# Kernel tuning notes

Measured on AMD Instinct MI355X. Metric: run time of the kernel, lower is better.

Reference implementation:

```python
import jax, jax.numpy as jnp
import numpy as np

N = 100000   # nodes
E = 1600000  # edges (avg degree 16)
F_IN = 64
H = 64
C = 40       # classes


def setup_inputs() -> dict:
    key = jax.random.key(0)
    ks = jax.random.split(key, 12)

    def lin(k, out_d, in_d):
        kw, kb = jax.random.split(k)
        W = jax.random.normal(kw, (out_d, in_d), jnp.float32) / jnp.sqrt(jnp.float32(in_d))
        b = jnp.zeros((out_d,), jnp.float32)
        return W, b

    Wl1, b1 = lin(ks[2], H, F_IN)
    Wr1, _ = lin(ks[3], H, F_IN)
    Wl2, b2 = lin(ks[4], H, H)
    Wr2, _ = lin(ks[5], H, H)
    Wl3, b3 = lin(ks[6], C, H)
    Wr3, _ = lin(ks[7], C, H)

    return {
        "x": jax.random.normal(ks[0], (N, F_IN), jnp.float32),
        "edge_index": jax.random.randint(ks[1], (2, E), 0, N, jnp.int32),
        "Wl1": Wl1, "Wr1": Wr1, "b1": b1,
        "Wl2": Wl2, "Wr2": Wr2, "b2": b2,
        "Wl3": Wl3, "Wr3": Wr3, "b3": b3,
    }


def _sage_conv(x, src, dst, Wl, Wr, b, n_nodes):
    # PyG SAGEConv (aggr='mean'): out = lin_l(mean_{j in N(i)} x_j) + lin_r(x_i)
    msg = x[src]                                                   # [E, F] gather
    agg_sum = jax.ops.segment_sum(msg, dst, num_segments=n_nodes)  # [N, F]
    deg = jax.ops.segment_sum(jnp.ones((src.shape[0],), x.dtype), dst,
                              num_segments=n_nodes)                # [N]
    agg = agg_sum / jnp.maximum(deg, 1.0)[:, None]                 # mean aggregation
    return agg @ Wl.T + b + x @ Wr.T


def reference(x, edge_index, Wl1, Wr1, b1, Wl2, Wr2, b2, Wl3, Wr3, b3):
    src, dst = edge_index[0], edge_index[1]
    n = x.shape[0]
    # dropout is identity in eval mode (training=self.training)
    h = jax.nn.relu(_sage_conv(x, src, dst, Wl1, Wr1, b1, n))
    h = jax.nn.relu(_sage_conv(h, src, dst, Wl2, Wr2, b2, n))
    h = _sage_conv(h, src, dst, Wl3, Wr3, b3, n)
    return jax.nn.log_softmax(h, axis=1)
```

## Files before the change

kernel.cpp:

```cpp
#include <hip/hip_runtime.h>
#include <hip/hip_bf16.h>
#include <math.h>


#define BK_SHIFT 7
#define BK_NODES 128
#define NB_MAX   1024

typedef __attribute__((ext_vector_type(8))) short short8;
typedef __attribute__((ext_vector_type(4))) float f32x4;

__device__ inline float blo(unsigned v) { union { unsigned u; float f; } c; c.u = v << 16; return c.f; }
__device__ inline float bhi(unsigned v) { union { unsigned u; float f; } c; c.u = v & 0xFFFF0000u; return c.f; }
__device__ inline unsigned short f2bf(float f) {
    union { float f; unsigned u; } c; c.f = f;
    unsigned r = (c.u + 0x7FFFu + ((c.u >> 16) & 1u)) >> 16;
    return (unsigned short)r;
}

__global__ __launch_bounds__(256) void bcount_kernel(const int* __restrict__ dstA,
                                                     int* __restrict__ bcount, int E, int NB) {
    __shared__ int lc[NB_MAX];
    int t = threadIdx.x;
    for (int i = t; i < NB; i += 256) lc[i] = 0;
    __syncthreads();
    int step = gridDim.x * 256;
    for (int e = blockIdx.x * 256 + t; e < E; e += step)
        atomicAdd(&lc[dstA[e] >> BK_SHIFT], 1);
    __syncthreads();
    for (int i = t; i < NB; i += 256)
        if (lc[i]) atomicAdd(&bcount[i], lc[i]);
}

__global__ __launch_bounds__(1024) void bscan_kernel(const int* __restrict__ bcount,
                                                     int* __restrict__ bbase,
                                                     int* __restrict__ cursor, int NB, int E) {
    __shared__ int s[1024];
    int t = threadIdx.x;
    int v = (t < NB) ? bcount[t] : 0;
    s[t] = v;
    __syncthreads();
    for (int off = 1; off < 1024; off <<= 1) {
        int x = 0;
        if (t >= off) x = s[t - off];
        __syncthreads();
        s[t] += x;
        __syncthreads();
    }
    if (t < NB) {
        int ex = s[t] - v;
        bbase[t] = ex;
        cursor[t] = ex;
    }
    if (t == 0) bbase[NB] = E;
}

__global__ __launch_bounds__(256) void bin_kernel(const int* __restrict__ srcA,
                                                  const int* __restrict__ dstA,
                                                  int* __restrict__ cursor,
                                                  int* __restrict__ binned, int E, int NB) {
    __shared__ int lc[NB_MAX];
    __shared__ int lbase[NB_MAX];
    int t = threadIdx.x;
    int chunk = (E + gridDim.x - 1) / gridDim.x;
    int e0 = blockIdx.x * chunk;
    int e1 = min(E, e0 + chunk);
    for (int i = t; i < NB; i += 256) lc[i] = 0;
    __syncthreads();
    for (int e = e0 + t; e < e1; e += 256)
        atomicAdd(&lc[dstA[e] >> BK_SHIFT], 1);
    __syncthreads();
    for (int i = t; i < NB; i += 256) {
        int c = lc[i];
        lbase[i] = c ? atomicAdd(&cursor[i], c) : 0;
    }
    __syncthreads();
    for (int i = t; i < NB; i += 256) lc[i] = 0;
    __syncthreads();
    for (int e = e0 + t; e < e1; e += 256) {
        int d = dstA[e];
        int b = d >> BK_SHIFT;
        int r = atomicAdd(&lc[b], 1);
        binned[lbase[b] + r] = srcA[e] | ((d & (BK_NODES - 1)) << 24);
    }
}

__global__ __launch_bounds__(256) void bsort_kernel(const int* __restrict__ binned,
                                                    const int* __restrict__ bbase,
                                                    int* __restrict__ col,
                                                    int* __restrict__ row_start, int N) {
    __shared__ int cnt[BK_NODES];
    __shared__ int base[BK_NODES];
    __shared__ int s[BK_NODES];
    int b = blockIdx.x, t = threadIdx.x;
    int e0 = bbase[b], e1 = bbase[b + 1];
    if (t < BK_NODES) cnt[t] = 0;
    __syncthreads();
    for (int e = e0 + t; e < e1; e += 256)
        atomicAdd(&cnt[(unsigned)binned[e] >> 24], 1);
    __syncthreads();
    int v = (t < BK_NODES) ? cnt[t] : 0;
    if (t < BK_NODES) s[t] = v;
    __syncthreads();
    for (int off = 1; off < BK_NODES; off <<= 1) {
        int x = 0;
        if (t < BK_NODES && t >= off) x = s[t - off];
        __syncthreads();
        if (t < BK_NODES) s[t] += x;
        __syncthreads();
    }
    if (t < BK_NODES) {
        base[t] = e0 + s[t] - v;
        int node = b * BK_NODES + t;
        if (node < N) row_start[node] = base[t];
        cnt[t] = 0;
    }
    if (b == gridDim.x - 1 && t == 0) row_start[N] = e1;
    __syncthreads();
    for (int e = e0 + t; e < e1; e += 256) {
        unsigned p = (unsigned)binned[e];
        int dl = p >> 24;
        int pos = base[dl] + atomicAdd(&cnt[dl], 1);
        col[pos] = p & 0xFFFFFF;
    }
}

__global__ __launch_bounds__(256) void xconv_kernel(const float* __restrict__ x,
                                                    unsigned short* __restrict__ Xb, int n8) {
    int i = blockIdx.x * 256 + threadIdx.x;
    if (i >= n8) return;
    const float* p = x + (size_t)i * 8;
    float4 a = *(const float4*)p;
    float4 b = *(const float4*)(p + 4);
    uint4 o;
    o.x = f2bf(a.x) | ((unsigned)f2bf(a.y) << 16);
    o.y = f2bf(a.z) | ((unsigned)f2bf(a.w) << 16);
    o.z = f2bf(b.x) | ((unsigned)f2bf(b.y) << 16);
    o.w = f2bf(b.z) | ((unsigned)f2bf(b.w) << 16);
    *(uint4*)(Xb + (size_t)i * 8) = o;
}

__global__ __launch_bounds__(256) void wconv_kernel(const float* __restrict__ Wl1, const float* __restrict__ Wr1,
                                                    const float* __restrict__ Wl2, const float* __restrict__ Wr2,
                                                    const float* __restrict__ Wl3, const float* __restrict__ Wr3,
                                                    unsigned short* __restrict__ Wb1,
                                                    unsigned short* __restrict__ Wb2,
                                                    unsigned short* __restrict__ Wb3) {
    int i = blockIdx.x * 256 + threadIdx.x;
    if (i < 8192) {
        int c = i >> 7, k = i & 127;
        float v = (k < 64) ? Wl1[c * 64 + k] : Wr1[c * 64 + k - 64];
        Wb1[i] = f2bf(v);
    } else if (i < 16384) {
        int j = i - 8192;
        int c = j >> 7, k = j & 127;
        float v = (k < 64) ? Wl2[c * 64 + k] : Wr2[c * 64 + k - 64];
        Wb2[j] = f2bf(v);
    } else if (i < 22528) {
        int j = i - 16384;
        int c = j >> 6, k = j & 63;
        float v = 0.f;
        if (c < 40) v = Wl3[c * 64 + k];
        else if (c >= 48 && c < 88) v = Wr3[(c - 48) * 64 + k];
        Wb3[j] = f2bf(v);
    }
}

__global__ __launch_bounds__(256) void agg64_kernel(const unsigned short* __restrict__ X,
                                                    const int* __restrict__ rs,
                                                    const int* __restrict__ col,
                                                    unsigned short* __restrict__ OUT, int n) {
    int t = threadIdx.x;
    int node = blockIdx.x * 16 + (t >> 4);
    if (node >= n) return;
    int lane = t & 15;
    int s = rs[node], d = rs[node + 1] - s;
    const unsigned short* lp = X + lane * 4;
    float ax = 0.f, ay = 0.f, az = 0.f, aw = 0.f;
    int j = 0;
    for (; j + 3 < d; j += 4) {
        int c0 = col[s + j], c1 = col[s + j + 1];
        int c2 = col[s + j + 2], c3 = col[s + j + 3];
        uint2 q0 = *(const uint2*)(lp + (size_t)c0 * 64);
        uint2 q1 = *(const uint2*)(lp + (size_t)c1 * 64);
        uint2 q2 = *(const uint2*)(lp + (size_t)c2 * 64);
        uint2 q3 = *(const uint2*)(lp + (size_t)c3 * 64);
        ax += (blo(q0.x) + blo(q1.x)) + (blo(q2.x) + blo(q3.x));
        ay += (bhi(q0.x) + bhi(q1.x)) + (bhi(q2.x) + bhi(q3.x));
        az += (blo(q0.y) + blo(q1.y)) + (blo(q2.y) + blo(q3.y));
        aw += (bhi(q0.y) + bhi(q1.y)) + (bhi(q2.y) + bhi(q3.y));
    }
    for (; j < d; ++j) {
        int c0 = col[s + j];
        uint2 q0 = *(const uint2*)(lp + (size_t)c0 * 64);
        ax += blo(q0.x); ay += bhi(q0.x); az += blo(q0.y); aw += bhi(q0.y);
    }
    float w = 1.f / (float)(d > 0 ? d : 1);
    ax *= w; ay *= w; az *= w; aw *= w;
    uint2 o;
    o.x = f2bf(ax) | ((unsigned)f2bf(ay) << 16);
    o.y = f2bf(az) | ((unsigned)f2bf(aw) << 16);
    *(uint2*)(OUT + (size_t)node * 64 + lane * 4) = o;
}

__global__ __launch_bounds__(256) void linmfma12_kernel(const unsigned short* __restrict__ A,
                                                        const unsigned short* __restrict__ X,
                                                        const unsigned short* __restrict__ Wb,
                                                        const float* __restrict__ bias,
                                                        unsigned short* __restrict__ OUT,
                                                        int N) {
    __shared__ unsigned short Ys[64][136];
    __shared__ unsigned short Ws[64][136];
    int t = threadIdx.x;
    int rowbase = blockIdx.x * 64;
#pragma unroll
    for (int it = 0; it < 4; ++it) {
        int idx = it * 256 + t;
        int row = idx >> 4, c = idx & 15;
        int grow = rowbase + row;
        if (grow >= N) grow = N - 1;
        const unsigned short* src = (c < 8) ? (A + (size_t)grow * 64 + c * 8)
                                            : (X + (size_t)grow * 64 + (c - 8) * 8);
        *(short8*)&Ys[row][c * 8] = *(const short8*)src;
        *(short8*)&Ws[row][c * 8] = *(const short8*)(Wb + (size_t)row * 128 + c * 8);
    }
    __syncthreads();
    int l = t & 63, w = t >> 6;
    int lrow = l & 15, lk = l >> 4;
    f32x4 acc0 = {0.f, 0.f, 0.f, 0.f};
    f32x4 acc1 = acc0, acc2 = acc0, acc3 = acc0;
#pragma unroll
    for (int kk = 0; kk < 4; ++kk) {
        int ko = kk * 32 + lk * 8;
        short8 a  = *(const short8*)&Ys[16 * w + lrow][ko];
        short8 b0 = *(const short8*)&Ws[lrow][ko];
        short8 b1 = *(const short8*)&Ws[16 + lrow][ko];
        short8 b2 = *(const short8*)&Ws[32 + lrow][ko];
        short8 b3 = *(const short8*)&Ws[48 + lrow][ko];
        acc0 = __builtin_amdgcn_mfma_f32_16x16x32_bf16(a, b0, acc0, 0, 0, 0);
        acc1 = __builtin_amdgcn_mfma_f32_16x16x32_bf16(a, b1, acc1, 0, 0, 0);
        acc2 = __builtin_amdgcn_mfma_f32_16x16x32_bf16(a, b2, acc2, 0, 0, 0);
        acc3 = __builtin_amdgcn_mfma_f32_16x16x32_bf16(a, b3, acc3, 0, 0, 0);
    }
#define EPI12(nt, accv)                                                   \
    {                                                                     \
        int colc = 16 * (nt) + lrow;                                      \
        float bv = bias[colc];                                            \
        _Pragma("unroll") for (int i = 0; i < 4; ++i) {                   \
            int grow = rowbase + 16 * w + lk * 4 + i;                     \
            if (grow < N) {                                               \
                float v = fmaxf(accv[i] + bv, 0.f);                       \
                OUT[(size_t)grow * 64 + colc] = f2bf(v);                  \
            }                                                             \
        }                                                                 \
    }
    EPI12(0, acc0) EPI12(1, acc1) EPI12(2, acc2) EPI12(3, acc3)
#undef EPI12
}

__global__ __launch_bounds__(256) void linmfma3_kernel(const unsigned short* __restrict__ H,
                                                       const unsigned short* __restrict__ Wb3,
                                                       const float* __restrict__ b3,
                                                       unsigned short* __restrict__ Z,
                                                       float* __restrict__ R,
                                                       int N) {
    __shared__ unsigned short Ys[64][72];
    __shared__ unsigned short Ws[96][72];
    int t = threadIdx.x;
    int rowbase = blockIdx.x * 64;
#pragma unroll
    for (int it = 0; it < 2; ++it) {
        int idx = it * 256 + t;
        int row = idx >> 3, c = idx & 7;
        int grow = rowbase + row;
        if (grow >= N) grow = N - 1;
        *(short8*)&Ys[row][c * 8] = *(const short8*)(H + (size_t)grow * 64 + c * 8);
    }
#pragma unroll
    for (int it = 0; it < 3; ++it) {
        int idx = it * 256 + t;
        int row = idx >> 3, c = idx & 7;
        *(short8*)&Ws[row][c * 8] = *(const short8*)(Wb3 + (size_t)row * 64 + c * 8);
    }
    __syncthreads();
    int l = t & 63, w = t >> 6;
    int lrow = l & 15, lk = l >> 4;
    f32x4 acc0 = {0.f, 0.f, 0.f, 0.f};
    f32x4 acc1 = acc0, acc2 = acc0, acc3 = acc0, acc4 = acc0, acc5 = acc0;
#pragma unroll
    for (int kk = 0; kk < 2; ++kk) {
        int ko = kk * 32 + lk * 8;
        short8 a  = *(const short8*)&Ys[16 * w + lrow][ko];
        short8 b0 = *(const short8*)&Ws[lrow][ko];
        short8 b1 = *(const short8*)&Ws[16 + lrow][ko];
        short8 b2 = *(const short8*)&Ws[32 + lrow][ko];
        short8 b3f = *(const short8*)&Ws[48 + lrow][ko];
        short8 b4 = *(const short8*)&Ws[64 + lrow][ko];
        short8 b5 = *(const short8*)&Ws[80 + lrow][ko];
        acc0 = __builtin_amdgcn_mfma_f32_16x16x32_bf16(a, b0, acc0, 0, 0, 0);
        acc1 = __builtin_amdgcn_mfma_f32_16x16x32_bf16(a, b1, acc1, 0, 0, 0);
        acc2 = __builtin_amdgcn_mfma_f32_16x16x32_bf16(a, b2, acc2, 0, 0, 0);
        acc3 = __builtin_amdgcn_mfma_f32_16x16x32_bf16(a, b3f, acc3, 0, 0, 0);
        acc4 = __builtin_amdgcn_mfma_f32_16x16x32_bf16(a, b4, acc4, 0, 0, 0);
        acc5 = __builtin_amdgcn_mfma_f32_16x16x32_bf16(a, b5, acc5, 0, 0, 0);
    }
#define EPI3(nt, accv)                                                     \
    {                                                                      \
        int colc = 16 * (nt) + lrow;                                       \
        _Pragma("unroll") for (int i = 0; i < 4; ++i) {                    \
            int grow = rowbase + 16 * w + lk * 4 + i;                      \
            if (grow < N) {                                                \
                float v = accv[i];                                         \
                if (colc < 40) {                                           \
                    Z[(size_t)grow * 40 + colc] = f2bf(v);                 \
                } else if (colc >= 48 && colc < 88) {                      \
                    R[(size_t)grow * 40 + (colc - 48)] = v + b3[colc - 48];\
                }                                                          \
            }                                                              \
        }                                                                  \
    }
    EPI3(0, acc0) EPI3(1, acc1) EPI3(2, acc2) EPI3(3, acc3) EPI3(4, acc4) EPI3(5, acc5)
#undef EPI3
}

__global__ __launch_bounds__(256) void agg40lsm_kernel(const unsigned short* __restrict__ Z,
                                                       const int* __restrict__ rs,
                                                       const int* __restrict__ col,
                                                       float* __restrict__ out, int n) {
    int t = threadIdx.x;
    int node = blockIdx.x * 16 + (t >> 4);
    if (node >= n) return;
    int lane = t & 15;
    bool act = lane < 10;
    int s = rs[node], d = rs[node + 1] - s;
    const unsigned short* lp = Z + lane * 4;
    float ax = 0.f, ay = 0.f, az = 0.f, aw = 0.f;
    int j = 0;
    for (; j + 3 < d; j += 4) {
        int c0 = col[s + j], c1 = col[s + j + 1];
        int c2 = col[s + j + 2], c3 = col[s + j + 3];
        if (act) {
            uint2 q0 = *(const uint2*)(lp + (size_t)c0 * 40);
            uint2 q1 = *(const uint2*)(lp + (size_t)c1 * 40);
            uint2 q2 = *(const uint2*)(lp + (size_t)c2 * 40);
            uint2 q3 = *(const uint2*)(lp + (size_t)c3 * 40);
            ax += (blo(q0.x) + blo(q1.x)) + (blo(q2.x) + blo(q3.x));
            ay += (bhi(q0.x) + bhi(q1.x)) + (bhi(q2.x) + bhi(q3.x));
            az += (blo(q0.y) + blo(q1.y)) + (blo(q2.y) + blo(q3.y));
            aw += (bhi(q0.y) + bhi(q1.y)) + (bhi(q2.y) + bhi(q3.y));
        }
    }
    for (; j < d; ++j) {
        int c0 = col[s + j];
        if (act) {
            uint2 q0 = *(const uint2*)(lp + (size_t)c0 * 40);
            ax += blo(q0.x); ay += bhi(q0.x); az += blo(q0.y); aw += bhi(q0.y);
        }
    }
    float w = 1.f / (float)(d > 0 ? d : 1);
    if (act) {
        float4 rv = *(const float4*)(out + (size_t)node * 40 + lane * 4);
        ax = ax * w + rv.x; ay = ay * w + rv.y;
        az = az * w + rv.z; aw = aw * w + rv.w;
    }
    float mx = act ? fmaxf(fmaxf(ax, ay), fmaxf(az, aw)) : -3.4e38f;
#pragma unroll
    for (int off = 1; off < 16; off <<= 1) mx = fmaxf(mx, __shfl_xor(mx, off, 16));
    float ssum = act ? (expf(ax - mx) + expf(ay - mx) + expf(az - mx) + expf(aw - mx)) : 0.f;
#pragma unroll
    for (int off = 1; off < 16; off <<= 1) ssum += __shfl_xor(ssum, off, 16);
    float lg = mx + logf(ssum);
    if (act) {
        float4 o;
        o.x = ax - lg; o.y = ay - lg; o.z = az - lg; o.w = aw - lg;
        *(float4*)(out + (size_t)node * 40 + lane * 4) = o;
    }
}

extern "C" void kernel_launch(void* const* d_in, const int* in_sizes, int n_in,
                              void* d_out, int out_size, void* d_ws, size_t ws_size,
                              hipStream_t stream) {
    const float* x   = (const float*)d_in[0];
    const int*   ei  = (const int*)d_in[1];
    const float* Wl1 = (const float*)d_in[2];
    const float* Wr1 = (const float*)d_in[3];
    const float* b1  = (const float*)d_in[4];
    const float* Wl2 = (const float*)d_in[5];
    const float* Wr2 = (const float*)d_in[6];
    const float* b2  = (const float*)d_in[7];
    const float* Wl3 = (const float*)d_in[8];
    const float* Wr3 = (const float*)d_in[9];
    const float* b3  = (const float*)d_in[10];
    float* out = (float*)d_out;

    const int N = in_sizes[0] / 64;
    const int E = in_sizes[1] / 2;
    const int NB = (N + BK_NODES - 1) / BK_NODES;
    const int* srcA = ei;
    const int* dstA = ei + E;

    char* ws = (char*)d_ws;
    size_t off = 0;
    auto alloc = [&](size_t bytes) {
        off = (off + 255) & ~(size_t)255;
        char* p = ws + off;
        off += bytes;
        return p;
    };
    int* bcount    = (int*)alloc((size_t)(NB_MAX + 1) * 4);
    int* bbase     = (int*)alloc((size_t)(NB_MAX + 1) * 4);
    int* cursor    = (int*)alloc((size_t)NB_MAX * 4);
    int* binned    = (int*)alloc((size_t)E * 4);
    int* col       = (int*)alloc((size_t)E * 4);
    int* row_start = (int*)alloc((size_t)(N + 1) * 4);
    unsigned short* Xb  = (unsigned short*)alloc((size_t)N * 64 * 2);
    unsigned short* AGG = (unsigned short*)alloc((size_t)N * 64 * 2);
    unsigned short* Hb  = (unsigned short*)alloc((size_t)N * 64 * 2);
    unsigned short* Zb  = (unsigned short*)alloc((size_t)N * 40 * 2);
    unsigned short* Wb1 = (unsigned short*)alloc(8192 * 2);
    unsigned short* Wb2 = (unsigned short*)alloc(8192 * 2);
    unsigned short* Wb3 = (unsigned short*)alloc(6144 * 2);

    hipMemsetAsync(bcount, 0, (size_t)(NB + 1) * 4, stream);
    bcount_kernel<<<256, 256, 0, stream>>>(dstA, bcount, E, NB);
    bscan_kernel<<<1, 1024, 0, stream>>>(bcount, bbase, cursor, NB, E);
    bin_kernel<<<128, 256, 0, stream>>>(srcA, dstA, cursor, binned, E, NB);
    bsort_kernel<<<NB, 256, 0, stream>>>(binned, bbase, col, row_start, N);

    xconv_kernel<<<(N * 64 / 8 + 255) / 256, 256, 0, stream>>>(x, Xb, N * 64 / 8);
    wconv_kernel<<<88, 256, 0, stream>>>(Wl1, Wr1, Wl2, Wr2, Wl3, Wr3, Wb1, Wb2, Wb3);

    int gridM = (N + 63) / 64;

    agg64_kernel<<<(N + 15) / 16, 256, 0, stream>>>(Xb, row_start, col, AGG, N);
    linmfma12_kernel<<<gridM, 256, 0, stream>>>(AGG, Xb, Wb1, b1, Hb, N);

    agg64_kernel<<<(N + 15) / 16, 256, 0, stream>>>(Hb, row_start, col, AGG, N);
    linmfma12_kernel<<<gridM, 256, 0, stream>>>(AGG, Hb, Wb2, b2, Hb, N);

    linmfma3_kernel<<<gridM, 256, 0, stream>>>(Hb, Wb3, b3, Zb, out, N);
    agg40lsm_kernel<<<(N + 15) / 16, 256, 0, stream>>>(Zb, row_start, col, out, N);
}
```

Measured before the change: 312.9 us.

## Fuse neighbor aggregation into SAGE linear kernel and merge prep kernels

Merges bucket counting, weight conversion and feature bf16 conversion into one prep kernel launch. Fuses mean aggregation of layers 1 and 2 directly into the MFMA linear kernel, writing aggregated rows into shared memory instead of round-tripping an AGG buffer through global memory. It uses 128-row tiles with 512 threads and separate H1/H2 buffers so the second layer no longer writes to its own input. It also raises the bin kernel grid size. This removes launches and a global write/read of the aggregate, at the cost of larger blocks and more shared memory per block.

```diff
diff --git a/kernel.cpp b/kernel.cpp
--- a/kernel.cpp
+++ b/kernel.cpp
@@ -18,18 +18,57 @@
     return (unsigned short)r;
 }
 
-__global__ __launch_bounds__(256) void bcount_kernel(const int* __restrict__ dstA,
-                                                     int* __restrict__ bcount, int E, int NB) {
-    __shared__ int lc[NB_MAX];
-    int t = threadIdx.x;
-    for (int i = t; i < NB; i += 256) lc[i] = 0;
-    __syncthreads();
-    int step = gridDim.x * 256;
-    for (int e = blockIdx.x * 256 + t; e < E; e += step)
-        atomicAdd(&lc[dstA[e] >> BK_SHIFT], 1);
-    __syncthreads();
-    for (int i = t; i < NB; i += 256)
-        if (lc[i]) atomicAdd(&bcount[i], lc[i]);
+__global__ __launch_bounds__(256) void prep_kernel(const int* __restrict__ dstA, int* __restrict__ bcount,
+                                                   int E, int NB,
+                                                   const float* __restrict__ x, unsigned short* __restrict__ Xb, int n8,
+                                                   const float* __restrict__ Wl1, const float* __restrict__ Wr1,
+                                                   const float* __restrict__ Wl2, const float* __restrict__ Wr2,
+                                                   const float* __restrict__ Wl3, const float* __restrict__ Wr3,
+                                                   unsigned short* __restrict__ Wb1,
+                                                   unsigned short* __restrict__ Wb2,
+                                                   unsigned short* __restrict__ Wb3) {
+    int b = blockIdx.x, t = threadIdx.x;
+    if (b < 256) {
+        __shared__ int lc[NB_MAX];
+        for (int i = t; i < NB; i += 256) lc[i] = 0;
+        __syncthreads();
+        for (int e = b * 256 + t; e < E; e += 256 * 256)
+            atomicAdd(&lc[dstA[e] >> BK_SHIFT], 1);
+        __syncthreads();
+        for (int i = t; i < NB; i += 256)
+            if (lc[i]) atomicAdd(&bcount[i], lc[i]);
+    } else if (b < 344) {
+        int i = (b - 256) * 256 + t;
+        if (i < 8192) {
+            int c = i >> 7, k = i & 127;
+            float v = (k < 64) ? Wl1[c * 64 + k] : Wr1[c * 64 + k - 64];
+            Wb1[i] = f2bf(v);
+        } else if (i < 16384) {
+            int j = i - 8192;
+            int c = j >> 7, k = j & 127;
+            float v = (k < 64) ? Wl2[c * 64 + k] : Wr2[c * 64 + k - 64];
+            Wb2[j] = f2bf(v);
+        } else if (i < 22528) {
+            int j = i - 16384;
+            int c = j >> 6, k = j & 63;
+            float v = 0.f;
+            if (c < 40) v = Wl3[c * 64 + k];
+            else if (c >= 48 && c < 88) v = Wr3[(c - 48) * 64 + k];
+            Wb3[j] = f2bf(v);
+        }
+    } else {
+        for (int i = (b - 344) * 256 + t; i < n8; i += 1024 * 256) {
+            const float* p = x + (size_t)i * 8;
+            float4 a = *(const float4*)p;
+            float4 bq = *(const float4*)(p + 4);
+            uint4 o;
+            o.x = f2bf(a.x) | ((unsigned)f2bf(a.y) << 16);
+            o.y = f2bf(a.z) | ((unsigned)f2bf(a.w) << 16);
+            o.z = f2bf(bq.x) | ((unsigned)f2bf(bq.y) << 16);
+            o.w = f2bf(bq.z) | ((unsigned)f2bf(bq.w) << 16);
+            *(uint4*)(Xb + (size_t)i * 8) = o;
+        }
+    }
 }
 
 __global__ __launch_bounds__(1024) void bscan_kernel(const int* __restrict__ bcount,
@@ -125,104 +164,67 @@
     }
 }
 
-__global__ __launch_bounds__(256) void xconv_kernel(const float* __restrict__ x,
-                                                    unsigned short* __restrict__ Xb, int n8) {
-    int i = blockIdx.x * 256 + threadIdx.x;
-    if (i >= n8) return;
-    const float* p = x + (size_t)i * 8;
-    float4 a = *(const float4*)p;
-    float4 b = *(const float4*)(p + 4);
-    uint4 o;
-    o.x = f2bf(a.x) | ((unsigned)f2bf(a.y) << 16);
-    o.y = f2bf(a.z) | ((unsigned)f2bf(a.w) << 16);
-    o.z = f2bf(b.x) | ((unsigned)f2bf(b.y) << 16);
-    o.w = f2bf(b.z) | ((unsigned)f2bf(b.w) << 16);
-    *(uint4*)(Xb + (size_t)i * 8) = o;
-}
-
-__global__ __launch_bounds__(256) void wconv_kernel(const float* __restrict__ Wl1, const float* __restrict__ Wr1,
-                                                    const float* __restrict__ Wl2, const float* __restrict__ Wr2,
-                                                    const float* __restrict__ Wl3, const float* __restrict__ Wr3,
-                                                    unsigned short* __restrict__ Wb1,
-                                                    unsigned short* __restrict__ Wb2,
-                                                    unsigned short* __restrict__ Wb3) {
-    int i = blockIdx.x * 256 + threadIdx.x;
-    if (i < 8192) {
-        int c = i >> 7, k = i & 127;
-        float v = (k < 64) ? Wl1[c * 64 + k] : Wr1[c * 64 + k - 64];
-        Wb1[i] = f2bf(v);
-    } else if (i < 16384) {
-        int j = i - 8192;
-        int c = j >> 7, k = j & 127;
-        float v = (k < 64) ? Wl2[c * 64 + k] : Wr2[c * 64 + k - 64];
-        Wb2[j] = f2bf(v);
-    } else if (i < 22528) {
-        int j = i - 16384;
-        int c = j >> 6, k = j & 63;
-        float v = 0.f;
-        if (c < 40) v = Wl3[c * 64 + k];
-        else if (c >= 48 && c < 88) v = Wr3[(c - 48) * 64 + k];
-        Wb3[j] = f2bf(v);
-    }
-}
-
-__global__ __launch_bounds__(256) void agg64_kernel(const unsigned short* __restrict__ X,
-                                                    const int* __restrict__ rs,
-                                                    const int* __restrict__ col,
-                                                    unsigned short* __restrict__ OUT, int n) {
-    int t = threadIdx.x;
-    int node = blockIdx.x * 16 + (t >> 4);
-    if (node >= n) return;
-    int lane = t & 15;
-    int s = rs[node], d = rs[node + 1] - s;
-    const unsigned short* lp = X + lane * 4;
-    float ax = 0.f, ay = 0.f, az = 0.f, aw = 0.f;
-    int j = 0;
-    for (; j + 3 < d; j += 4) {
-        int c0 = col[s + j], c1 = col[s + j + 1];
-        int c2 = col[s + j + 2], c3 = col[s + j + 3];
-        uint2 q0 = *(const uint2*)(lp + (size_t)c0 * 64);
-        uint2 q1 = *(const uint2*)(lp + (size_t)c1 * 64);
-        uint2 q2 = *(const uint2*)(lp + (size_t)c2 * 64);
-        uint2 q3 = *(const uint2*)(lp + (size_t)c3 * 64);
-        ax += (blo(q0.x) + blo(q1.x)) + (blo(q2.x) + blo(q3.x));
-        ay += (bhi(q0.x) + bhi(q1.x)) + (bhi(q2.x) + bhi(q3.x));
-        az += (blo(q0.y) + blo(q1.y)) + (blo(q2.y) + blo(q3.y));
-        aw += (bhi(q0.y) + bhi(q1.y)) + (bhi(q2.y) + bhi(q3.y));
-    }
-    for (; j < d; ++j) {
-        int c0 = col[s + j];
-        uint2 q0 = *(const uint2*)(lp + (size_t)c0 * 64);
-        ax += blo(q0.x); ay += bhi(q0.x); az += blo(q0.y); aw += bhi(q0.y);
-    }
-    float w = 1.f / (float)(d > 0 ? d : 1);
-    ax *= w; ay *= w; az *= w; aw *= w;
-    uint2 o;
-    o.x = f2bf(ax) | ((unsigned)f2bf(ay) << 16);
-    o.y = f2bf(az) | ((unsigned)f2bf(aw) << 16);
-    *(uint2*)(OUT + (size_t)node * 64 + lane * 4) = o;
-}
-
-__global__ __launch_bounds__(256) void linmfma12_kernel(const unsigned short* __restrict__ A,
-                                                        const unsigned short* __restrict__ X,
-                                                        const unsigned short* __restrict__ Wb,
-                                                        const float* __restrict__ bias,
-                                                        unsigned short* __restrict__ OUT,
-                                                        int N) {
-    __shared__ unsigned short Ys[64][136];
+__global__ __launch_bounds__(512) void sage12_kernel(const unsigned short* __restrict__ X,
+                                                     const unsigned short* __restrict__ Wb,
+                                                     const float* __restrict__ bias,
+                                                     const int* __restrict__ rs,
+                                                     const int* __restrict__ col,
+                                                     unsigned short* __restrict__ OUT,
+                                                     int N) {
+    __shared__ unsigned short Ys[128][136];
     __shared__ unsigned short Ws[64][136];
     int t = threadIdx.x;
-    int rowbase = blockIdx.x * 64;
-#pragma unroll
-    for (int it = 0; it < 4; ++it) {
-        int idx = it * 256 + t;
+    int rowbase = blockIdx.x * 128;
+#pragma unroll
+    for (int it = 0; it < 2; ++it) {
+        int idx = it * 512 + t;
         int row = idx >> 4, c = idx & 15;
+        *(short8*)&Ws[row][c * 8] = *(const short8*)(Wb + (size_t)row * 128 + c * 8);
+    }
+#pragma unroll
+    for (int it = 0; it < 2; ++it) {
+        int idx = it * 512 + t;
+        int row = idx >> 3, c = idx & 7;
         int grow = rowbase + row;
         if (grow >= N) grow = N - 1;
-        const unsigned short* src = (c < 8) ? (A + (size_t)grow * 64 + c * 8)
-                                            : (X + (size_t)grow * 64 + (c - 8) * 8);
-        *(short8*)&Ys[row][c * 8] = *(const short8*)src;
-        *(short8*)&Ws[row][c * 8] = *(const short8*)(Wb + (size_t)row * 128 + c * 8);
+        *(short8*)&Ys[row][64 + c * 8] = *(const short8*)(X + (size_t)grow * 64 + c * 8);
+    }
+    {
+        int g = t >> 4, lane = t & 15;
+        const unsigned short* lp = X + lane * 4;
+#pragma unroll
+        for (int k = 0; k < 4; ++k) {
+            int row = g + k * 32;
+            int node = rowbase + row;
+            float ax = 0.f, ay = 0.f, az = 0.f, aw = 0.f;
+            if (node < N) {
+                int s = rs[node], d = rs[node + 1] - s;
+                int j = 0;
+                for (; j + 3 < d; j += 4) {
+                    int c0 = col[s + j], c1 = col[s + j + 1];
+                    int c2 = col[s + j + 2], c3 = col[s + j + 3];
+                    uint2 q0 = *(const uint2*)(lp + (size_t)c0 * 64);
+                    uint2 q1 = *(const uint2*)(lp + (size_t)c1 * 64);
+                    uint2 q2 = *(const uint2*)(lp + (size_t)c2 * 64);
+                    uint2 q3 = *(const uint2*)(lp + (size_t)c3 * 64);
+                    ax += (blo(q0.x) + blo(q1.x)) + (blo(q2.x) + blo(q3.x));
+                    ay += (bhi(q0.x) + bhi(q1.x)) + (bhi(q2.x) + bhi(q3.x));
+                    az += (blo(q0.y) + blo(q1.y)) + (blo(q2.y) + blo(q3.y));
+                    aw += (bhi(q0.y) + bhi(q1.y)) + (bhi(q2.y) + bhi(q3.y));
+                }
+                for (; j < d; ++j) {
+                    int c0 = col[s + j];
+                    uint2 q0 = *(const uint2*)(lp + (size_t)c0 * 64);
+                    ax += blo(q0.x); ay += bhi(q0.x); az += blo(q0.y); aw += bhi(q0.y);
+                }
+                float w = 1.f / (float)(d > 0 ? d : 1);
+                ax *= w; ay *= w; az *= w; aw *= w;
+            }
+            uint2 o;
+            o.x = f2bf(ax) | ((unsigned)f2bf(ay) << 16);
+            o.y = f2bf(az) | ((unsigned)f2bf(aw) << 16);
+            *(uint2*)&Ys[row][lane * 4] = o;
+        }
     }
     __syncthreads();
     int l = t & 63, w = t >> 6;
@@ -414,30 +416,24 @@
     int* col       = (int*)alloc((size_t)E * 4);
     int* row_start = (int*)alloc((size_t)(N + 1) * 4);
     unsigned short* Xb  = (unsigned short*)alloc((size_t)N * 64 * 2);
-    unsigned short* AGG = (unsigned short*)alloc((size_t)N * 64 * 2);
-    unsigned short* Hb  = (unsigned short*)alloc((size_t)N * 64 * 2);
+    unsigned short* H1  = (unsigned short*)alloc((size_t)N * 64 * 2);
+    unsigned short* H2  = (unsigned short*)alloc((size_t)N * 64 * 2);
     unsigned short* Zb  = (unsigned short*)alloc((size_t)N * 40 * 2);
     unsigned short* Wb1 = (unsigned short*)alloc(8192 * 2);
     unsigned short* Wb2 = (unsigned short*)alloc(8192 * 2);
     unsigned short* Wb3 = (unsigned short*)alloc(6144 * 2);
 
     hipMemsetAsync(bcount, 0, (size_t)(NB + 1) * 4, stream);
-    bcount_kernel<<<256, 256, 0, stream>>>(dstA, bcount, E, NB);
+    prep_kernel<<<1368, 256, 0, stream>>>(dstA, bcount, E, NB, x, Xb, N * 64 / 8,
+                                          Wl1, Wr1, Wl2, Wr2, Wl3, Wr3, Wb1, Wb2, Wb3);
     bscan_kernel<<<1, 1024, 0, stream>>>(bcount, bbase, cursor, NB, E);
-    bin_kernel<<<128, 256, 0, stream>>>(srcA, dstA, cursor, binned, E, NB);
+    bin_kernel<<<512, 256, 0, stream>>>(srcA, dstA, cursor, binned, E, NB);
     bsort_kernel<<<NB, 256, 0, stream>>>(binned, bbase, col, row_start, N);
 
-    xconv_kernel<<<(N * 64 / 8 + 255) / 256, 256, 0, stream>>>(x, Xb, N * 64 / 8);
-    wconv_kernel<<<88, 256, 0, stream>>>(Wl1, Wr1, Wl2, Wr2, Wl3, Wr3, Wb1, Wb2, Wb3);
-
-    int gridM = (N + 63) / 64;
-
-    agg64_kernel<<<(N + 15) / 16, 256, 0, stream>>>(Xb, row_start, col, AGG, N);
-    linmfma12_kernel<<<gridM, 256, 0, stream>>>(AGG, Xb, Wb1, b1, Hb, N);
-
-    agg64_kernel<<<(N + 15) / 16, 256, 0, stream>>>(Hb, row_start, col, AGG, N);
-    linmfma12_kernel<<<gridM, 256, 0, stream>>>(AGG, Hb, Wb2, b2, Hb, N);
-
-    linmfma3_kernel<<<gridM, 256, 0, stream>>>(Hb, Wb3, b3, Zb, out, N);
+    int grid128 = (N + 127) / 128;
+    sage12_kernel<<<grid128, 512, 0, stream>>>(Xb, Wb1, b1, row_start, col, H1, N);
+    sage12_kernel<<<grid128, 512, 0, stream>>>(H1, Wb2, b2, row_start, col, H2, N);
+
+    linmfma3_kernel<<<(N + 63) / 64, 256, 0, stream>>>(H2, Wb3, b3, Zb, out, N);
     agg40lsm_kernel<<<(N + 15) / 16, 256, 0, stream>>>(Zb, row_start, col, out, N);
 }
```

Result: slower. 322.1 us (+3.0%).

## Widen neighbor gathers to 16-byte loads and fuse preprocessing kernels

Applied to the files above, without the earlier changes.

Aggregation kernels now assign 8 lanes per node with 16-byte bf16 loads instead of 16 lanes with 8-byte loads, doubling nodes per block and halving shuffle width in the softmax reduction. The bucket count, x conversion and weight conversion kernels are merged into one launch partitioned by block index. The binning kernel grid is enlarged. This aims to cut per-edge load instruction count and launch overhead, at the cost of fewer active lanes per row in the 40-wide case.

```diff
diff --git a/kernel.cpp b/kernel.cpp
--- a/kernel.cpp
+++ b/kernel.cpp
@@ -18,18 +18,57 @@
     return (unsigned short)r;
 }
 
-__global__ __launch_bounds__(256) void bcount_kernel(const int* __restrict__ dstA,
-                                                     int* __restrict__ bcount, int E, int NB) {
-    __shared__ int lc[NB_MAX];
-    int t = threadIdx.x;
-    for (int i = t; i < NB; i += 256) lc[i] = 0;
-    __syncthreads();
-    int step = gridDim.x * 256;
-    for (int e = blockIdx.x * 256 + t; e < E; e += step)
-        atomicAdd(&lc[dstA[e] >> BK_SHIFT], 1);
-    __syncthreads();
-    for (int i = t; i < NB; i += 256)
-        if (lc[i]) atomicAdd(&bcount[i], lc[i]);
+__global__ __launch_bounds__(256) void prep_kernel(const int* __restrict__ dstA, int* __restrict__ bcount,
+                                                   int E, int NB,
+                                                   const float* __restrict__ x, unsigned short* __restrict__ Xb, int n8,
+                                                   const float* __restrict__ Wl1, const float* __restrict__ Wr1,
+                                                   const float* __restrict__ Wl2, const float* __restrict__ Wr2,
+                                                   const float* __restrict__ Wl3, const float* __restrict__ Wr3,
+                                                   unsigned short* __restrict__ Wb1,
+                                                   unsigned short* __restrict__ Wb2,
+                                                   unsigned short* __restrict__ Wb3) {
+    int b = blockIdx.x, t = threadIdx.x;
+    if (b < 256) {
+        __shared__ int lc[NB_MAX];
+        for (int i = t; i < NB; i += 256) lc[i] = 0;
+        __syncthreads();
+        for (int e = b * 256 + t; e < E; e += 256 * 256)
+            atomicAdd(&lc[dstA[e] >> BK_SHIFT], 1);
+        __syncthreads();
+        for (int i = t; i < NB; i += 256)
+            if (lc[i]) atomicAdd(&bcount[i], lc[i]);
+    } else if (b < 344) {
+        int i = (b - 256) * 256 + t;
+        if (i < 8192) {
+            int c = i >> 7, k = i & 127;
+            float v = (k < 64) ? Wl1[c * 64 + k] : Wr1[c * 64 + k - 64];
+            Wb1[i] = f2bf(v);
+        } else if (i < 16384) {
+            int j = i - 8192;
+            int c = j >> 7, k = j & 127;
+            float v = (k < 64) ? Wl2[c * 64 + k] : Wr2[c * 64 + k - 64];
+            Wb2[j] = f2bf(v);
+        } else if (i < 22528) {
+            int j = i - 16384;
+            int c = j >> 6, k = j & 63;
+            float v = 0.f;
+            if (c < 40) v = Wl3[c * 64 + k];
+            else if (c >= 48 && c < 88) v = Wr3[(c - 48) * 64 + k];
+            Wb3[j] = f2bf(v);
+        }
+    } else {
+        for (int i = (b - 344) * 256 + t; i < n8; i += 1024 * 256) {
+            const float* p = x + (size_t)i * 8;
+            float4 a = *(const float4*)p;
+            float4 bq = *(const float4*)(p + 4);
+            uint4 o;
+            o.x = f2bf(a.x) | ((unsigned)f2bf(a.y) << 16);
+            o.y = f2bf(a.z) | ((unsigned)f2bf(a.w) << 16);
+            o.z = f2bf(bq.x) | ((unsigned)f2bf(bq.y) << 16);
+            o.w = f2bf(bq.z) | ((unsigned)f2bf(bq.w) << 16);
+            *(uint4*)(Xb + (size_t)i * 8) = o;
+        }
+    }
 }
 
 __global__ __launch_bounds__(1024) void bscan_kernel(const int* __restrict__ bcount,
@@ -125,82 +164,48 @@
     }
 }
 
-__global__ __launch_bounds__(256) void xconv_kernel(const float* __restrict__ x,
-                                                    unsigned short* __restrict__ Xb, int n8) {
-    int i = blockIdx.x * 256 + threadIdx.x;
-    if (i >= n8) return;
-    const float* p = x + (size_t)i * 8;
-    float4 a = *(const float4*)p;
-    float4 b = *(const float4*)(p + 4);
-    uint4 o;
-    o.x = f2bf(a.x) | ((unsigned)f2bf(a.y) << 16);
-    o.y = f2bf(a.z) | ((unsigned)f2bf(a.w) << 16);
-    o.z = f2bf(b.x) | ((unsigned)f2bf(b.y) << 16);
-    o.w = f2bf(b.z) | ((unsigned)f2bf(b.w) << 16);
-    *(uint4*)(Xb + (size_t)i * 8) = o;
-}
-
-__global__ __launch_bounds__(256) void wconv_kernel(const float* __restrict__ Wl1, const float* __restrict__ Wr1,
-                                                    const float* __restrict__ Wl2, const float* __restrict__ Wr2,
-                                                    const float* __restrict__ Wl3, const float* __restrict__ Wr3,
-                                                    unsigned short* __restrict__ Wb1,
-                                                    unsigned short* __restrict__ Wb2,
-                                                    unsigned short* __restrict__ Wb3) {
-    int i = blockIdx.x * 256 + threadIdx.x;
-    if (i < 8192) {
-        int c = i >> 7, k = i & 127;
-        float v = (k < 64) ? Wl1[c * 64 + k] : Wr1[c * 64 + k - 64];
-        Wb1[i] = f2bf(v);
-    } else if (i < 16384) {
-        int j = i - 8192;
-        int c = j >> 7, k = j & 127;
-        float v = (k < 64) ? Wl2[c * 64 + k] : Wr2[c * 64 + k - 64];
-        Wb2[j] = f2bf(v);
-    } else if (i < 22528) {
-        int j = i - 16384;
-        int c = j >> 6, k = j & 63;
-        float v = 0.f;
-        if (c < 40) v = Wl3[c * 64 + k];
-        else if (c >= 48 && c < 88) v = Wr3[(c - 48) * 64 + k];
-        Wb3[j] = f2bf(v);
-    }
-}
-
 __global__ __launch_bounds__(256) void agg64_kernel(const unsigned short* __restrict__ X,
                                                     const int* __restrict__ rs,
                                                     const int* __restrict__ col,
                                                     unsigned short* __restrict__ OUT, int n) {
     int t = threadIdx.x;
-    int node = blockIdx.x * 16 + (t >> 4);
+    int node = blockIdx.x * 32 + (t >> 3);
     if (node >= n) return;
-    int lane = t & 15;
+    int lane = t & 7;
     int s = rs[node], d = rs[node + 1] - s;
-    const unsigned short* lp = X + lane * 4;
-    float ax = 0.f, ay = 0.f, az = 0.f, aw = 0.f;
+    const unsigned short* lp = X + lane * 8;
+    float a0 = 0.f, a1 = 0.f, a2 = 0.f, a3 = 0.f, a4 = 0.f, a5 = 0.f, a6 = 0.f, a7 = 0.f;
     int j = 0;
     for (; j + 3 < d; j += 4) {
         int c0 = col[s + j], c1 = col[s + j + 1];
         int c2 = col[s + j + 2], c3 = col[s + j + 3];
-        uint2 q0 = *(const uint2*)(lp + (size_t)c0 * 64);
-        uint2 q1 = *(const uint2*)(lp + (size_t)c1 * 64);
-        uint2 q2 = *(const uint2*)(lp + (size_t)c2 * 64);
-        uint2 q3 = *(const uint2*)(lp + (size_t)c3 * 64);
-        ax += (blo(q0.x) + blo(q1.x)) + (blo(q2.x) + blo(q3.x));
-        ay += (bhi(q0.x) + bhi(q1.x)) + (bhi(q2.x) + bhi(q3.x));
-        az += (blo(q0.y) + blo(q1.y)) + (blo(q2.y) + blo(q3.y));
-        aw += (bhi(q0.y) + bhi(q1.y)) + (bhi(q2.y) + bhi(q3.y));
+        uint4 q0 = *(const uint4*)(lp + (size_t)c0 * 64);
+        uint4 q1 = *(const uint4*)(lp + (size_t)c1 * 64);
+        uint4 q2 = *(const uint4*)(lp + (size_t)c2 * 64);
+        uint4 q3 = *(const uint4*)(lp + (size_t)c3 * 64);
+        a0 += (blo(q0.x) + blo(q1.x)) + (blo(q2.x) + blo(q3.x));
+        a1 += (bhi(q0.x) + bhi(q1.x)) + (bhi(q2.x) + bhi(q3.x));
+        a2 += (blo(q0.y) + blo(q1.y)) + (blo(q2.y) + blo(q3.y));
+        a3 += (bhi(q0.y) + bhi(q1.y)) + (bhi(q2.y) + bhi(q3.y));
+        a4 += (blo(q0.z) + blo(q1.z)) + (blo(q2.z) + blo(q3.z));
+        a5 += (bhi(q0.z) + bhi(q1.z)) + (bhi(q2.z) + bhi(q3.z));
+        a6 += (blo(q0.w) + blo(q1.w)) + (blo(q2.w) + blo(q3.w));
+        a7 += (bhi(q0.w) + bhi(q1.w)) + (bhi(q2.w) + bhi(q3.w));
     }
     for (; j < d; ++j) {
         int c0 = col[s + j];
-        uint2 q0 = *(const uint2*)(lp + (size_t)c0 * 64);
-        ax += blo(q0.x); ay += bhi(q0.x); az += blo(q0.y); aw += bhi(q0.y);
+        uint4 q0 = *(const uint4*)(lp + (size_t)c0 * 64);
+        a0 += blo(q0.x); a1 += bhi(q0.x); a2 += blo(q0.y); a3 += bhi(q0.y);
+        a4 += blo(q0.z); a5 += bhi(q0.z); a6 += blo(q0.w); a7 += bhi(q0.w);
     }
     float w = 1.f / (float)(d > 0 ? d : 1);
-    ax *= w; ay *= w; az *= w; aw *= w;
-    uint2 o;
-    o.x = f2bf(ax) | ((unsigned)f2bf(ay) << 16);
-    o.y = f2bf(az) | ((unsigned)f2bf(aw) << 16);
-    *(uint2*)(OUT + (size_t)node * 64 + lane * 4) = o;
+    a0 *= w; a1 *= w; a2 *= w; a3 *= w; a4 *= w; a5 *= w; a6 *= w; a7 *= w;
+    uint4 o;
+    o.x = f2bf(a0) | ((unsigned)f2bf(a1) << 16);
+    o.y = f2bf(a2) | ((unsigned)f2bf(a3) << 16);
+    o.z = f2bf(a4) | ((unsigned)f2bf(a5) << 16);
+    o.w = f2bf(a6) | ((unsigned)f2bf(a7) << 16);
+    *(uint4*)(OUT + (size_t)node * 64 + lane * 8) = o;
 }
 
 __global__ __launch_bounds__(256) void linmfma12_kernel(const unsigned short* __restrict__ A,
@@ -328,52 +333,64 @@
                                                        const int* __restrict__ col,
                                                        float* __restrict__ out, int n) {
     int t = threadIdx.x;
-    int node = blockIdx.x * 16 + (t >> 4);
+    int node = blockIdx.x * 32 + (t >> 3);
     if (node >= n) return;
-    int lane = t & 15;
-    bool act = lane < 10;
+    int lane = t & 7;
+    bool act = lane < 5;
     int s = rs[node], d = rs[node + 1] - s;
-    const unsigned short* lp = Z + lane * 4;
-    float ax = 0.f, ay = 0.f, az = 0.f, aw = 0.f;
+    const unsigned short* lp = Z + lane * 8;
+    float a0 = 0.f, a1 = 0.f, a2 = 0.f, a3 = 0.f, a4 = 0.f, a5 = 0.f, a6 = 0.f, a7 = 0.f;
     int j = 0;
     for (; j + 3 < d; j += 4) {
         int c0 = col[s + j], c1 = col[s + j + 1];
         int c2 = col[s + j + 2], c3 = col[s + j + 3];
         if (act) {
-            uint2 q0 = *(const uint2*)(lp + (size_t)c0 * 40);
-            uint2 q1 = *(const uint2*)(lp + (size_t)c1 * 40);
-            uint2 q2 = *(const uint2*)(lp + (size_t)c2 * 40);
-            uint2 q3 = *(const uint2*)(lp + (size_t)c3 * 40);
-            ax += (blo(q0.x) + blo(q1.x)) + (blo(q2.x) + blo(q3.x));
-            ay += (bhi(q0.x) + bhi(q1.x)) + (bhi(q2.x) + bhi(q3.x));
-            az += (blo(q0.y) + blo(q1.y)) + (blo(q2.y) + blo(q3.y));
-            aw += (bhi(q0.y) + bhi(q1.y)) + (bhi(q2.y) + bhi(q3.y));
+            uint4 q0 = *(const uint4*)(lp + (size_t)c0 * 40);
+            uint4 q1 = *(const uint4*)(lp + (size_t)c1 * 40);
+            uint4 q2 = *(const uint4*)(lp + (size_t)c2 * 40);
+            uint4 q3 = *(const uint4*)(lp + (size_t)c3 * 40);
+            a0 += (blo(q0.x) + blo(q1.x)) + (blo(q2.x) + blo(q3.x));
+            a1 += (bhi(q0.x) + bhi(q1.x)) + (bhi(q2.x) + bhi(q3.x));
+            a2 += (blo(q0.y) + blo(q1.y)) + (blo(q2.y) + blo(q3.y));
+            a3 += (bhi(q0.y) + bhi(q1.y)) + (bhi(q2.y) + bhi(q3.y));
+            a4 += (blo(q0.z) + blo(q1.z)) + (blo(q2.z) + blo(q3.z));
+            a5 += (bhi(q0.z) + bhi(q1.z)) + (bhi(q2.z) + bhi(q3.z));
+            a6 += (blo(q0.w) + blo(q1.w)) + (blo(q2.w) + blo(q3.w));
+            a7 += (bhi(q0.w) + bhi(q1.w)) + (bhi(q2.w) + bhi(q3.w));
         }
     }
     for (; j < d; ++j) {
         int c0 = col[s + j];
         if (act) {
-            uint2 q0 = *(const uint2*)(lp + (size_t)c0 * 40);
-            ax += blo(q0.x); ay += bhi(q0.x); az += blo(q0.y); aw += bhi(q0.y);
+            uint4 q0 = *(const uint4*)(lp + (size_t)c0 * 40);
+            a0 += blo(q0.x); a1 += bhi(q0.x); a2 += blo(q0.y); a3 += bhi(q0.y);
+            a4 += blo(q0.z); a5 += bhi(q0.z); a6 += blo(q0.w); a7 += bhi(q0.w);
         }
     }
     float w = 1.f / (float)(d > 0 ? d : 1);
     if (act) {
-        float4 rv = *(const float4*)(out + (size_t)node * 40 + lane * 4);
-        ax = ax * w + rv.x; ay = ay * w + rv.y;
-        az = az * w + rv.z; aw = aw * w + rv.w;
-    }
-    float mx = act ? fmaxf(fmaxf(ax, ay), fmaxf(az, aw)) : -3.4e38f;
-#pragma unroll
-    for (int off = 1; off < 16; off <<= 1) mx = fmaxf(mx, __shfl_xor(mx, off, 16));
-    float ssum = act ? (expf(ax - mx) + expf(ay - mx) + expf(az - mx) + expf(aw - mx)) : 0.f;
-#pragma unroll
-    for (int off = 1; off < 16; off <<= 1) ssum += __shfl_xor(ssum, off, 16);
+        float* op = out + (size_t)node * 40 + lane * 8;
+        float4 r0 = *(const float4*)op;
+        float4 r1 = *(const float4*)(op + 4);
+        a0 = a0 * w + r0.x; a1 = a1 * w + r0.y; a2 = a2 * w + r0.z; a3 = a3 * w + r0.w;
+        a4 = a4 * w + r1.x; a5 = a5 * w + r1.y; a6 = a6 * w + r1.z; a7 = a7 * w + r1.w;
+    }
+    float mx = act ? fmaxf(fmaxf(fmaxf(a0, a1), fmaxf(a2, a3)),
+                           fmaxf(fmaxf(a4, a5), fmaxf(a6, a7))) : -3.4e38f;
+#pragma unroll
+    for (int off = 1; off < 8; off <<= 1) mx = fmaxf(mx, __shfl_xor(mx, off, 8));
+    float ssum = act ? (expf(a0 - mx) + expf(a1 - mx) + expf(a2 - mx) + expf(a3 - mx) +
+                        expf(a4 - mx) + expf(a5 - mx) + expf(a6 - mx) + expf(a7 - mx)) : 0.f;
+#pragma unroll
+    for (int off = 1; off < 8; off <<= 1) ssum += __shfl_xor(ssum, off, 8);
     float lg = mx + logf(ssum);
     if (act) {
-        float4 o;
-        o.x = ax - lg; o.y = ay - lg; o.z = az - lg; o.w = aw - lg;
-        *(float4*)(out + (size_t)node * 40 + lane * 4) = o;
+        float* op = out + (size_t)node * 40 + lane * 8;
+        float4 o0, o1;
+        o0.x = a0 - lg; o0.y = a1 - lg; o0.z = a2 - lg; o0.w = a3 - lg;
+        o1.x = a4 - lg; o1.y = a5 - lg; o1.z = a6 - lg; o1.w = a7 - lg;
+        *(float4*)op = o0;
+        *(float4*)(op + 4) = o1;
     }
 }
 
@@ -422,22 +439,21 @@
     unsigned short* Wb3 = (unsigned short*)alloc(6144 * 2);
 
     hipMemsetAsync(bcount, 0, (size_t)(NB + 1) * 4, stream);
-    bcount_kernel<<<256, 256, 0, stream>>>(dstA, bcount, E, NB);
+    prep_kernel<<<1368, 256, 0, stream>>>(dstA, bcount, E, NB, x, Xb, N * 64 / 8,
+                                          Wl1, Wr1, Wl2, Wr2, Wl3, Wr3, Wb1, Wb2, Wb3);
     bscan_kernel<<<1, 1024, 0, stream>>>(bcount, bbase, cursor, NB, E);
-    bin_kernel<<<128, 256, 0, stream>>>(srcA, dstA, cursor, binned, E, NB);
+    bin_kernel<<<512, 256, 0, stream>>>(srcA, dstA, cursor, binned, E, NB);
     bsort_kernel<<<NB, 256, 0, stream>>>(binned, bbase, col, row_start, N);
 
-    xconv_kernel<<<(N * 64 / 8 + 255) / 256, 256, 0, stream>>>(x, Xb, N * 64 / 8);
-    wconv_kernel<<<88, 256, 0, stream>>>(Wl1, Wr1, Wl2, Wr2, Wl3, Wr3, Wb1, Wb2, Wb3);
-
+    int gridA = (N + 31) / 32;
     int gridM = (N + 63) / 64;
 
-    agg64_kernel<<<(N + 15) / 16, 256, 0, stream>>>(Xb, row_start, col, AGG, N);
+    agg64_kernel<<<gridA, 256, 0, stream>>>(Xb, row_start, col, AGG, N);
     linmfma12_kernel<<<gridM, 256, 0, stream>>>(AGG, Xb, Wb1, b1, Hb, N);
 
-    agg64_kernel<<<(N + 15) / 16, 256, 0, stream>>>(Hb, row_start, col, AGG, N);
+    agg64_kernel<<<gridA, 256, 0, stream>>>(Hb, row_start, col, AGG, N);
     linmfma12_kernel<<<gridM, 256, 0, stream>>>(AGG, Hb, Wb2, b2, Hb, N);
 
     linmfma3_kernel<<<gridM, 256, 0, stream>>>(Hb, Wb3, b3, Zb, out, N);
-    agg40lsm_kernel<<<(N + 15) / 16, 256, 0, stream>>>(Zb, row_start, col, out, N);
-}
+    agg40lsm_kernel<<<gridA, 256, 0, stream>>>(Zb, row_start, col, out, N);
+}
```

Measured after the change: 285.0 us. 8.9% less time.
